# Performance work log

Measured on AMD Instinct MI355X. Metric: run time of the kernel, lower is better.

The kernel has to match this reference:

```python
import jax, jax.numpy as jnp
import numpy as np

B, T = 64, 512
N_EMB, HIDDEN, VOCAB = 768, 256, 3072


def setup_inputs() -> dict:
    key = jax.random.key(0)
    ks = jax.random.split(key, 5)
    def xavier(k, shape):
        bound = float(np.sqrt(6.0 / (shape[0] + shape[1])))
        return jax.random.uniform(k, shape, jnp.float32, -bound, bound)
    return {
        "idx": jax.random.randint(ks[0], (B, T), 0, VOCAB),
        "emb_table": jax.random.normal(ks[1], (VOCAB, N_EMB), jnp.float32),
        "Wxh": xavier(ks[2], (N_EMB, HIDDEN)),
        "Whh": xavier(ks[3], (HIDDEN, HIDDEN)),
        "Wy": xavier(ks[4], (HIDDEN, VOCAB)),
        "By": jnp.zeros((VOCAB,), jnp.float32),
        "Bh": jnp.zeros((HIDDEN,), jnp.float32),
    }


def reference(idx, emb_table, Wxh, Whh, Wy, By, Bh):
    # embedded: [B, T, E] -> scan over time with hidden carry [B, H]
    embedded = emb_table[idx]                      # gather
    xWxh = jnp.einsum('bte,eh->tbh', embedded, Wxh)  # precompute input projection

    def step(hidden, x_t):
        hidden = jnp.tanh(x_t + hidden @ Whh + Bh)
        return hidden, None

    h0 = jnp.zeros((idx.shape[0], Whh.shape[0]), embedded.dtype)
    hidden, _ = jax.lax.scan(step, h0, xWxh)
    # return_sequences=False: only the last step's output is returned
    out = hidden @ Wy + By
    return out, hidden
```

## Files before the change

kernel.cpp:

```cpp
#include <hip/hip_runtime.h>
#include <hip/hip_bf16.h>

typedef _Float16 half8 __attribute__((ext_vector_type(8)));
typedef float f32x4 __attribute__((ext_vector_type(4)));

#define B_SZ 64
#define T_SZ 512
#define E_SZ 768
#define H_SZ 256
#define V_SZ 3072

#define WS_P     0u
#define WS_WT    16777216u
#define WS_WF    17170432u
#define WS_H     17301504u

static __device__ __forceinline__ float fast_tanh(float x) {
  float e = __builtin_amdgcn_exp2f(x * 2.8853900817779268f);
  return 1.0f - 2.0f * __builtin_amdgcn_rcpf(1.0f + e);
}

__global__ __launch_bounds__(256) void k0_convert(
    const float* __restrict__ Wxh,
    const float* __restrict__ Whh,
    _Float16* __restrict__ Wtf,
    _Float16* __restrict__ Wf)
{
  int gid = blockIdx.x * 256 + threadIdx.x;
  if (gid < E_SZ * H_SZ) {
    int e = gid >> 8, n = gid & 255;
    float v = Wxh[gid];
    int ki = e >> 5, kb = (e >> 3) & 3, j = e & 7;
    int f  = ((n >> 4) << 6) | (kb << 4) | (n & 15);
    Wtf[(size_t)ki * 8192 + (size_t)f * 8 + j] = (_Float16)v;
  }
  if (gid < 65536) {
    int row = gid >> 8, col = gid & 255;
    float v = Whh[gid];
    int kt = row >> 5, quad = (row >> 3) & 3, j = row & 7;
    int nt = col >> 4;
    int lane = (quad << 4) | (col & 15);
    Wf[(((size_t)(nt * 8 + kt) * 64 + lane) * 8) + j] = (_Float16)v;
  }
}

__global__ __launch_bounds__(256) void k1_xproj(
    const float* __restrict__ emb,
    const _Float16* __restrict__ Wtf,
    _Float16* __restrict__ P)
{
  const int tid  = threadIdx.x;
  const int w    = tid >> 6;
  const int lane = tid & 63;
  const int m16  = lane & 15;
  const int quad = lane >> 4;
  const int r = blockIdx.x * 64 + w * 16 + m16;
  const float* Arow = emb + (size_t)r * E_SZ + quad * 8;

  __shared__ __align__(16) _Float16 bp[2][16 * 64 * 8];
  uint4 stg[4];
#pragma unroll
  for (int pp = 0; pp < 4; ++pp)
    stg[pp] = *(const uint4*)(Wtf + (size_t)(tid + 256 * pp) * 8);
  f32x4 af0 = *(const f32x4*)(Arow);
  f32x4 af1 = *(const f32x4*)(Arow + 4);

  f32x4 acc[16];
#pragma unroll
  for (int n = 0; n < 16; ++n) { f32x4 z = {0.f, 0.f, 0.f, 0.f}; acc[n] = z; }

#pragma unroll
  for (int pp = 0; pp < 4; ++pp)
    *(uint4*)(bp[0] + (size_t)(tid + 256 * pp) * 8) = stg[pp];
  __syncthreads();

#pragma unroll 1
  for (int ki = 0; ki < 24; ++ki) {
    const _Float16* cur = bp[ki & 1];
    f32x4 af0n = af0, af1n = af1;
    if (ki < 23) {
#pragma unroll
      for (int pp = 0; pp < 4; ++pp)
        stg[pp] = *(const uint4*)(Wtf + (size_t)(ki + 1) * 8192
                                      + (size_t)(tid + 256 * pp) * 8);
      af0n = *(const f32x4*)(Arow + (ki + 1) * 32);
      af1n = *(const f32x4*)(Arow + (ki + 1) * 32 + 4);
    }
    half8 a;
#pragma unroll
    for (int e = 0; e < 4; ++e) { a[e] = (_Float16)af0[e]; a[4 + e] = (_Float16)af1[e]; }
#pragma unroll
    for (int nt = 0; nt < 16; ++nt) {
      half8 bb = *(const half8*)(cur + (size_t)(nt * 64 + lane) * 8);
      acc[nt] = __builtin_amdgcn_mfma_f32_16x16x32_f16(a, bb, acc[nt], 0, 0, 0);
    }
    if (ki < 23) {
#pragma unroll
      for (int pp = 0; pp < 4; ++pp)
        *(uint4*)(bp[(ki + 1) & 1] + (size_t)(tid + 256 * pp) * 8) = stg[pp];
      __syncthreads();
    }
    af0 = af0n; af1 = af1n;
  }
  const int rbase = blockIdx.x * 64 + w * 16 + quad * 4;
#pragma unroll
  for (int nt = 0; nt < 16; ++nt) {
    const int col = nt * 16 + m16;
#pragma unroll
    for (int rg = 0; rg < 4; ++rg) {
      P[(size_t)(rbase + rg) * H_SZ + col] = (_Float16)acc[nt][rg];
    }
  }
}

#define LDFRAG(C, KT, R0, R1, R2, R3) { \
  uint4 q = Wf4[(((size_t)(w * 4 + C) * 8 + KT) * 64) + lane]; \
  asm volatile("v_accvgpr_write_b32 a" #R0 ", %0" :: "v"(q.x) : "a" #R0); \
  asm volatile("v_accvgpr_write_b32 a" #R1 ", %0" :: "v"(q.y) : "a" #R1); \
  asm volatile("v_accvgpr_write_b32 a" #R2 ", %0" :: "v"(q.z) : "a" #R2); \
  asm volatile("v_accvgpr_write_b32 a" #R3 ", %0" :: "v"(q.w) : "a" #R3); }

#define MFMA_K0(A0, Z) \
  asm volatile( \
    "v_mfma_f32_16x16x32_f16 %[t0], %[a], a[0:3],   %[z]\n\t" \
    "v_mfma_f32_16x16x32_f16 %[t1], %[a], a[32:35], %[z]\n\t" \
    "v_mfma_f32_16x16x32_f16 %[t2], %[a], a[64:67], %[z]\n\t" \
    "v_mfma_f32_16x16x32_f16 %[t3], %[a], a[96:99], %[z]" \
    : [t0] "=&v"(acc0), [t1] "=&v"(acc1), [t2] "=&v"(acc2), [t3] "=&v"(acc3) \
    : [a] "v"(A0), [z] "v"(Z));

#define MFMA_KT(A0, B0, B1, B2, B3) \
  asm volatile( \
    "v_mfma_f32_16x16x32_f16 %[t0], %[a], a[" #B0 "], %[t0]\n\t" \
    "v_mfma_f32_16x16x32_f16 %[t1], %[a], a[" #B1 "], %[t1]\n\t" \
    "v_mfma_f32_16x16x32_f16 %[t2], %[a], a[" #B2 "], %[t2]\n\t" \
    "v_mfma_f32_16x16x32_f16 %[t3], %[a], a[" #B3 "], %[t3]" \
    : [t0] "+v"(acc0), [t1] "+v"(acc1), [t2] "+v"(acc2), [t3] "+v"(acc3) \
    : [a] "v"(A0));

#define MFMA_K7(A0, B0, B1, B2, B3) \
  asm volatile( \
    "v_mfma_f32_16x16x32_f16 %[t0], %[a], a[" #B0 "], %[t0]\n\t" \
    "v_mfma_f32_16x16x32_f16 %[t1], %[a], a[" #B1 "], %[t1]\n\t" \
    "v_mfma_f32_16x16x32_f16 %[t2], %[a], a[" #B2 "], %[t2]\n\t" \
    "v_mfma_f32_16x16x32_f16 %[t3], %[a], a[" #B3 "], %[t3]\n\t" \
    "s_nop 7\n\t" \
    "s_nop 7" \
    : [t0] "+v"(acc0), [t1] "+v"(acc1), [t2] "+v"(acc2), [t3] "+v"(acc3) \
    : [a] "v"(A0));

__global__ __launch_bounds__(256) void k2_rnn(
    const _Float16* __restrict__ Wf,
    const _Float16* __restrict__ P,
    const int* __restrict__ idx,
    const float* __restrict__ Bh,
    float* __restrict__ hout,
    float* __restrict__ hidout)
{
  const int b    = blockIdx.x;
  const int tid  = threadIdx.x;
  const int w    = tid >> 6;
  const int lane = tid & 63;
  const int quad = lane >> 4;
  __shared__ __align__(16) _Float16 hb[2][H_SZ];
  const uint4* Wf4 = (const uint4*)Wf;

  LDFRAG(0,0,  0,  1,  2,  3)  LDFRAG(0,1,  4,  5,  6,  7)
  LDFRAG(0,2,  8,  9, 10, 11)  LDFRAG(0,3, 12, 13, 14, 15)
  LDFRAG(0,4, 16, 17, 18, 19)  LDFRAG(0,5, 20, 21, 22, 23)
  LDFRAG(0,6, 24, 25, 26, 27)  LDFRAG(0,7, 28, 29, 30, 31)
  LDFRAG(1,0, 32, 33, 34, 35)  LDFRAG(1,1, 36, 37, 38, 39)
  LDFRAG(1,2, 40, 41, 42, 43)  LDFRAG(1,3, 44, 45, 46, 47)
  LDFRAG(1,4, 48, 49, 50, 51)  LDFRAG(1,5, 52, 53, 54, 55)
  LDFRAG(1,6, 56, 57, 58, 59)  LDFRAG(1,7, 60, 61, 62, 63)
  LDFRAG(2,0, 64, 65, 66, 67)  LDFRAG(2,1, 68, 69, 70, 71)
  LDFRAG(2,2, 72, 73, 74, 75)  LDFRAG(2,3, 76, 77, 78, 79)
  LDFRAG(2,4, 80, 81, 82, 83)  LDFRAG(2,5, 84, 85, 86, 87)
  LDFRAG(2,6, 88, 89, 90, 91)  LDFRAG(2,7, 92, 93, 94, 95)
  LDFRAG(3,0, 96, 97, 98, 99)  LDFRAG(3,1,100,101,102,103)
  LDFRAG(3,2,104,105,106,107)  LDFRAG(3,3,108,109,110,111)
  LDFRAG(3,4,112,113,114,115)  LDFRAG(3,5,116,117,118,119)
  LDFRAG(3,6,120,121,122,123)  LDFRAG(3,7,124,125,126,127)

  const float bhj = Bh[tid];
  const int* idxb = idx + b * T_SZ;
  int rowA = idxb[2];
  int rowB = idxb[3];
  _Float16 xA = P[(size_t)idxb[0] * H_SZ + tid];
  _Float16 xB = P[(size_t)idxb[1] * H_SZ + tid];
  f32x4 zero4 = {0.f, 0.f, 0.f, 0.f};
  asm volatile("" : "+v"(zero4));
  hb[1][tid] = (_Float16)0.f;
  float hval = 0.f;
  __syncthreads();

#define K2_STEP(HR, HW, XV)                                              \
  {                                                                      \
    const _Float16* hr = (HR);                                           \
    half8 va0 = *(const half8*)(hr +   0 + quad * 8);                    \
    half8 va1 = *(const half8*)(hr +  32 + quad * 8);                    \
    half8 va2 = *(const half8*)(hr +  64 + quad * 8);                    \
    half8 va3 = *(const half8*)(hr +  96 + quad * 8);                    \
    half8 va4 = *(const half8*)(hr + 128 + quad * 8);                    \
    half8 va5 = *(const half8*)(hr + 160 + quad * 8);                    \
    half8 va6 = *(const half8*)(hr + 192 + quad * 8);                    \
    half8 va7 = *(const half8*)(hr + 224 + quad * 8);                    \
    f32x4 acc0, acc1, acc2, acc3;                                        \
    MFMA_K0(va0, zero4)                                                  \
    MFMA_KT(va1,   4:7,  36:39,  68:71, 100:103)                         \
    MFMA_KT(va2,  8:11,  40:43,  72:75, 104:107)                         \
    MFMA_KT(va3, 12:15,  44:47,  76:79, 108:111)                         \
    MFMA_KT(va4, 16:19,  48:51,  80:83, 112:115)                         \
    MFMA_KT(va5, 20:23,  52:55,  84:87, 116:119)                         \
    MFMA_KT(va6, 24:27,  56:59,  88:91, 120:123)                         \
    MFMA_K7(va7, 28:31,  60:63,  92:95, 124:127)                         \
    float v0 = acc0[0], v1 = acc1[0], v2 = acc2[0], v3 = acc3[0];        \
    float ylo = (quad & 1) ? v1 : v0;                                    \
    float yhi = (quad & 1) ? v3 : v2;                                    \
    float y   = (quad & 2) ? yhi : ylo;          \
    hval = fast_tanh(y + (XV) + bhj);                                    \
    (HW)[tid] = (_Float16)hval;                                          \
    __syncthreads();                                                     \
  }

#pragma unroll 1
  for (int tt = 0; tt < 256; ++tt) {
    float xvA = (float)xA;
    xA = P[(size_t)rowA * H_SZ + tid];
    int t4 = 2 * tt + 4; t4 = t4 > 511 ? 511 : t4;
    rowA = idxb[t4];
    K2_STEP(hb[1], hb[0], xvA)
    float xvB = (float)xB;
    xB = P[(size_t)rowB * H_SZ + tid];
    int t5 = 2 * tt + 5; t5 = t5 > 511 ? 511 : t5;
    rowB = idxb[t5];
    K2_STEP(hb[0], hb[1], xvB)
  }
#undef K2_STEP
  hout[b * H_SZ + tid] = hval;
  hidout[b * H_SZ + tid] = hval;
}

__global__ __launch_bounds__(256) void k3_out(
    const float* __restrict__ h,
    const float* __restrict__ Wy,
    const float* __restrict__ By,
    float* __restrict__ out)
{
  __shared__ float hs[H_SZ];
  const int c = blockIdx.x;
  const int b = blockIdx.y;
  const int v = c * 256 + threadIdx.x;
  hs[threadIdx.x] = h[b * H_SZ + threadIdx.x];
  __syncthreads();
  float a0 = By[v], a1 = 0.f, a2 = 0.f, a3 = 0.f;
#pragma unroll 4
  for (int jj = 0; jj < H_SZ; jj += 4) {
    a0 += hs[jj + 0] * Wy[(size_t)(jj + 0) * V_SZ + v];
    a1 += hs[jj + 1] * Wy[(size_t)(jj + 1) * V_SZ + v];
    a2 += hs[jj + 2] * Wy[(size_t)(jj + 2) * V_SZ + v];
    a3 += hs[jj + 3] * Wy[(size_t)(jj + 3) * V_SZ + v];
  }
  out[(size_t)b * V_SZ + v] = (a0 + a1) + (a2 + a3);
}

extern "C" void kernel_launch(void* const* d_in, const int* in_sizes, int n_in,
                              void* d_out, int out_size, void* d_ws, size_t ws_size,
                              hipStream_t stream)
{
  const int*   idx = (const int*)d_in[0];
  const float* emb = (const float*)d_in[1];
  const float* Wxh = (const float*)d_in[2];
  const float* Whh = (const float*)d_in[3];
  const float* Wy  = (const float*)d_in[4];
  const float* By  = (const float*)d_in[5];
  const float* Bh  = (const float*)d_in[6];

  char* ws = (char*)d_ws;
  _Float16* P    = (_Float16*)(ws + WS_P);
  _Float16* Wtf  = (_Float16*)(ws + WS_WT);
  _Float16* Wf   = (_Float16*)(ws + WS_WF);
  float*    hbuf = (float*)(ws + WS_H);

  float* out    = (float*)d_out;
  float* hidout = out + (size_t)B_SZ * V_SZ;

  k0_convert<<<768, 256, 0, stream>>>(Wxh, Whh, Wtf, Wf);
  k1_xproj  <<<48, 256, 0, stream>>>(emb, Wtf, P);
  k2_rnn    <<<64, 256, 0, stream>>>(Wf, P, idx, Bh, hbuf, hidout);
  k3_out    <<<dim3(12, 64), 256, 0, stream>>>(hbuf, Wy, By, out);
}
```

Before: 357.6 us.

## Fuse output projection into RNN kernel and stage indices in shared memory

Result: slower. 403.7 us (+12.9%).

```diff
diff --git a/kernel.cpp b/kernel.cpp
--- a/kernel.cpp
+++ b/kernel.cpp
@@ -13,7 +13,6 @@
 #define WS_P     0u
 #define WS_WT    16777216u
 #define WS_WF    17170432u
-#define WS_H     17301504u
 
 static __device__ __forceinline__ float fast_tanh(float x) {
   float e = __builtin_amdgcn_exp2f(x * 2.8853900817779268f);
@@ -154,7 +153,9 @@
     const _Float16* __restrict__ P,
     const int* __restrict__ idx,
     const float* __restrict__ Bh,
-    float* __restrict__ hout,
+    const float* __restrict__ Wy,
+    const float* __restrict__ By,
+    float* __restrict__ out,
     float* __restrict__ hidout)
 {
   const int b    = blockIdx.x;
@@ -163,6 +164,8 @@
   const int lane = tid & 63;
   const int quad = lane >> 4;
   __shared__ __align__(16) _Float16 hb[2][H_SZ];
+  __shared__ int   ids[520];
+  __shared__ float hf[H_SZ];
   const uint4* Wf4 = (const uint4*)Wf;
 
   LDFRAG(0,0,  0,  1,  2,  3)  LDFRAG(0,1,  4,  5,  6,  7)
@@ -184,6 +187,7 @@
 
   const float bhj = Bh[tid];
   const int* idxb = idx + b * T_SZ;
+  for (int i = tid; i < 520; i += 256) ids[i] = idxb[i < 512 ? i : 511];
   int rowA = idxb[2];
   int rowB = idxb[3];
   _Float16 xA = P[(size_t)idxb[0] * H_SZ + tid];
@@ -226,42 +230,32 @@
 #pragma unroll 1
   for (int tt = 0; tt < 256; ++tt) {
     float xvA = (float)xA;
-    xA = P[(size_t)rowA * H_SZ + tid];
-    int t4 = 2 * tt + 4; t4 = t4 > 511 ? 511 : t4;
-    rowA = idxb[t4];
+    xA = P[rowA * H_SZ + tid];
+    rowA = ids[2 * tt + 4];
     K2_STEP(hb[1], hb[0], xvA)
     float xvB = (float)xB;
-    xB = P[(size_t)rowB * H_SZ + tid];
-    int t5 = 2 * tt + 5; t5 = t5 > 511 ? 511 : t5;
-    rowB = idxb[t5];
+    xB = P[rowB * H_SZ + tid];
+    rowB = ids[2 * tt + 5];
     K2_STEP(hb[0], hb[1], xvB)
   }
 #undef K2_STEP
-  hout[b * H_SZ + tid] = hval;
   hidout[b * H_SZ + tid] = hval;
-}
-
-__global__ __launch_bounds__(256) void k3_out(
-    const float* __restrict__ h,
-    const float* __restrict__ Wy,
-    const float* __restrict__ By,
-    float* __restrict__ out)
-{
-  __shared__ float hs[H_SZ];
-  const int c = blockIdx.x;
-  const int b = blockIdx.y;
-  const int v = c * 256 + threadIdx.x;
-  hs[threadIdx.x] = h[b * H_SZ + threadIdx.x];
+
+  hf[tid] = hval;
   __syncthreads();
-  float a0 = By[v], a1 = 0.f, a2 = 0.f, a3 = 0.f;
+#pragma unroll 1
+  for (int c = 0; c < 12; ++c) {
+    const int v = c * 256 + tid;
+    float a0 = By[v], a1 = 0.f, a2 = 0.f, a3 = 0.f;
 #pragma unroll 4
-  for (int jj = 0; jj < H_SZ; jj += 4) {
-    a0 += hs[jj + 0] * Wy[(size_t)(jj + 0) * V_SZ + v];
-    a1 += hs[jj + 1] * Wy[(size_t)(jj + 1) * V_SZ + v];
-    a2 += hs[jj + 2] * Wy[(size_t)(jj + 2) * V_SZ + v];
-    a3 += hs[jj + 3] * Wy[(size_t)(jj + 3) * V_SZ + v];
-  }
-  out[(size_t)b * V_SZ + v] = (a0 + a1) + (a2 + a3);
+    for (int jj = 0; jj < H_SZ; jj += 4) {
+      a0 += hf[jj + 0] * Wy[(size_t)(jj + 0) * V_SZ + v];
+      a1 += hf[jj + 1] * Wy[(size_t)(jj + 1) * V_SZ + v];
+      a2 += hf[jj + 2] * Wy[(size_t)(jj + 2) * V_SZ + v];
+      a3 += hf[jj + 3] * Wy[(size_t)(jj + 3) * V_SZ + v];
+    }
+    out[(size_t)b * V_SZ + v] = (a0 + a1) + (a2 + a3);
+  }
 }
 
 extern "C" void kernel_launch(void* const* d_in, const int* in_sizes, int n_in,
@@ -280,13 +274,11 @@
   _Float16* P    = (_Float16*)(ws + WS_P);
   _Float16* Wtf  = (_Float16*)(ws + WS_WT);
   _Float16* Wf   = (_Float16*)(ws + WS_WF);
-  float*    hbuf = (float*)(ws + WS_H);
 
   float* out    = (float*)d_out;
   float* hidout = out + (size_t)B_SZ * V_SZ;
 
   k0_convert<<<768, 256, 0, stream>>>(Wxh, Whh, Wtf, Wf);
   k1_xproj  <<<48, 256, 0, stream>>>(emb, Wtf, P);
-  k2_rnn    <<<64, 256, 0, stream>>>(Wf, P, idx, Bh, hbuf, hidout);
-  k3_out    <<<dim3(12, 64), 256, 0, stream>>>(hbuf, Wy, By, out);
-}
+  k2_rnn    <<<64, 256, 0, stream>>>(Wf, P, idx, Bh, Wy, By, out, hidout);
+}
```
